# Kernel tuning notes

Hardware: AMD Instinct MI355X
Metric: run time of the kernel (lower is better)

## Reference

```python
import jax, jax.numpy as jnp
import numpy as np

NUM_CLASSES = 80
FOCAL_ALPHA = 0.25
FOCAL_GAMMA = 2.0
HUBER_SIGMA = 3.0
REG_MEAN = 0.0
REG_STD = 0.2
IMG_H = 800.0
IMG_W = 800.0
B, A, M = 4, 100000, 32


def setup_inputs() -> dict:
    key = jax.random.key(0)
    k1, k2, k3, k4, k5, k6, k7 = jax.random.split(key, 7)
    classification = jax.random.uniform(k1, (B, A, NUM_CLASSES), dtype=jnp.float32)
    regression = jax.random.normal(k2, (B, A, 4), dtype=jnp.float32)
    # plausible anchors: centers inside image, sizes 16..256
    cx = jax.random.uniform(k3, (A,), minval=0.0, maxval=IMG_W)
    cy = jax.random.uniform(k4, (A,), minval=0.0, maxval=IMG_H)
    s = jax.random.uniform(k5, (A, 2), minval=16.0, maxval=256.0)
    anchors = jnp.stack([cx - s[:, 0] / 2, cy - s[:, 1] / 2,
                         cx + s[:, 0] / 2, cy + s[:, 1] / 2], axis=1).astype(jnp.float32)
    # annotations: [B, M, 5] = x1,y1,x2,y2,class
    xy = jax.random.uniform(k6, (B, M, 2), minval=0.0, maxval=650.0)
    wh = jax.random.uniform(k7, (B, M, 2), minval=30.0, maxval=150.0)
    cls = jax.random.randint(jax.random.fold_in(key, 9), (B, M, 1), 0, NUM_CLASSES).astype(jnp.float32)
    annotations = jnp.concatenate([xy, xy + wh, cls], axis=-1)
    return {"classification": classification, "regression": regression,
            "anchors": anchors, "annotations": annotations}


def _pairwise_iou(anchors, boxes):
    # anchors [A,4], boxes [M,4] -> [A,M]
    ix1 = jnp.maximum(anchors[:, None, 0], boxes[None, :, 0])
    iy1 = jnp.maximum(anchors[:, None, 1], boxes[None, :, 1])
    ix2 = jnp.minimum(anchors[:, None, 2], boxes[None, :, 2])
    iy2 = jnp.minimum(anchors[:, None, 3], boxes[None, :, 3])
    inter = jnp.clip(ix2 - ix1, 0.0) * jnp.clip(iy2 - iy1, 0.0)
    area_a = (anchors[:, 2] - anchors[:, 0]) * (anchors[:, 3] - anchors[:, 1])
    area_b = (boxes[:, 2] - boxes[:, 0]) * (boxes[:, 3] - boxes[:, 1])
    union = area_a[:, None] + area_b[None, :] - inter
    return inter / jnp.maximum(union, 1e-8)


def _targets(anchors, annotations):
    # per-image anchor assignment, vmapped over batch
    def per_image(ann):
        boxes = ann[:, :4]
        cls = ann[:, 4].astype(jnp.int32)
        ious = _pairwise_iou(anchors, boxes)          # [A,M]
        best = jnp.argmax(ious, axis=1)               # [A]
        best_iou = jnp.max(ious, axis=1)
        pos = best_iou >= 0.5
        ign = (best_iou > 0.4) & (~pos)
        states = jnp.where(pos, 1.0, jnp.where(ign, -1.0, 0.0))
        cx = (anchors[:, 0] + anchors[:, 2]) * 0.5
        cy = (anchors[:, 1] + anchors[:, 3]) * 0.5
        inside = (cx >= 0) & (cx < IMG_W) & (cy >= 0) & (cy < IMG_H)
        states = jnp.where(inside, states, -1.0)
        labels = jax.nn.one_hot(cls[best], NUM_CLASSES, dtype=jnp.float32) * pos[:, None]
        ab = boxes[best]                              # assigned gt boxes [A,4]
        aw = anchors[:, 2] - anchors[:, 0]
        ah = anchors[:, 3] - anchors[:, 1]
        t = jnp.stack([(ab[:, 0] - anchors[:, 0]) / aw,
                       (ab[:, 1] - anchors[:, 1]) / ah,
                       (ab[:, 2] - anchors[:, 2]) / aw,
                       (ab[:, 3] - anchors[:, 3]) / ah], axis=1)
        t = (t - REG_MEAN) / REG_STD
        return labels, t, states
    return jax.vmap(per_image)(annotations)


def reference(classification, regression, anchors, annotations):
    labels, reg_t, states = _targets(anchors, annotations)   # [B,A,K],[B,A,4],[B,A]
    num_pos = jnp.maximum(jnp.sum((states == 1.0).astype(jnp.float32)), 1.0)
    # focal loss over non-ignored anchors
    valid = (states != -1.0)[..., None].astype(jnp.float32)
    p = jnp.clip(classification, 1e-4, 1.0 - 1e-4)
    bce = -(labels * jnp.log(p) + (1.0 - labels) * jnp.log1p(-p))
    alpha_f = jnp.where(labels == 1.0, FOCAL_ALPHA, 1.0 - FOCAL_ALPHA)
    focal_w = alpha_f * jnp.where(labels == 1.0, 1.0 - p, p) ** FOCAL_GAMMA
    cls_loss = jnp.sum(focal_w * bce * valid) / num_pos
    # smooth L1 over positive anchors
    pos_m = (states == 1.0)[..., None].astype(jnp.float32)
    s2 = HUBER_SIGMA ** 2
    d = jnp.abs(regression - reg_t)
    l1 = jnp.where(d < 1.0 / s2, 0.5 * s2 * d * d, d - 0.5 / s2)
    reg_loss = jnp.sum(l1 * pos_m) / num_pos
    return cls_loss + reg_loss
```

## Files before the change

kernel.cpp:

```cpp
#include <hip/hip_runtime.h>

#define BB 4
#define AA 100000
#define MM 32
#define NC 80
#define GX 391
#define NBLK (GX * BB)


#define FOCAL_K(vk, flatk)                                                  \
  {                                                                         \
    const int s    = (flatk) / 20;                                          \
    const int colb = ((flatk) - s * 20) * 4;                                \
    const int c    = scode[s];                                              \
    const float m  = (c != -2) ? 1.0f : 0.0f;                               \
    const float q0 = fminf(fmaxf((vk).x, 1e-4f), 0.9999f);                  \
    const float q1 = fminf(fmaxf((vk).y, 1e-4f), 0.9999f);                  \
    const float q2 = fminf(fmaxf((vk).z, 1e-4f), 0.9999f);                  \
    const float q3 = fminf(fmaxf((vk).w, 1e-4f), 0.9999f);                  \
    float sub = 0.0f;                                                       \
    sub += 0.75f * q0 * q0 * (-__logf(1.0f - q0));                          \
    sub += 0.75f * q1 * q1 * (-__logf(1.0f - q1));                          \
    sub += 0.75f * q2 * q2 * (-__logf(1.0f - q2));                          \
    sub += 0.75f * q3 * q3 * (-__logf(1.0f - q3));                          \
    csum += m * sub;                                                        \
    const unsigned rel = (unsigned)(c - colb);                              \
    if (rel < 4u) {      \
      const float p = (rel & 2u) ? ((rel & 1u) ? q3 : q2)                   \
                                 : ((rel & 1u) ? q1 : q0);                  \
      const float onem = 1.0f - p;                                          \
      csum += 0.25f * onem * onem * (-__logf(p))                            \
            - 0.75f * p * p * (-__logf(onem));                              \
    }                                                                       \
  }

#define FOCAL_BATCH(vv, batch)                                              \
  _Pragma("unroll")                                                         \
  for (int k = 0; k < 5; ++k) {                                             \
    const int flat = ((batch) * 5 + k) * 256 + tid;                         \
    FOCAL_K((vv)[k], flat)                                                  \
  }

__global__ __launch_bounds__(256, 4) void fused_kernel(
    const float* __restrict__ anchors,
    const float* __restrict__ annotations,
    const float* __restrict__ regression,
    const float* __restrict__ cls,
    float* __restrict__ cls_part,
    float* __restrict__ reg_part,
    unsigned* __restrict__ pos_part)
{
    __shared__ float ann[MM * 5];
    __shared__ float areab[MM];
    __shared__ int scode[256];
    const int b = blockIdx.y;
    const int tid = threadIdx.x;
    if (tid < MM * 5) ann[tid] = annotations[b * MM * 5 + tid];
    if (tid < MM) {
        const float bx1 = annotations[b * MM * 5 + tid * 5 + 0];
        const float by1 = annotations[b * MM * 5 + tid * 5 + 1];
        const float bx2 = annotations[b * MM * 5 + tid * 5 + 2];
        const float by2 = annotations[b * MM * 5 + tid * 5 + 3];
        areab[tid] = __fmul_rn(__fsub_rn(bx2, bx1), __fsub_rn(by2, by1));
    }
    __syncthreads();

    const int abase = blockIdx.x * 256;
    const int a = abase + tid;

    const float4* base4 = (const float4*)cls + ((size_t)b * AA + abase) * 20;
    const int maxflat = (abase + 256 <= AA) ? (5120 - 1) : ((AA - abase) * 20 - 1);

    float4 vA[5], vB[5];
    #pragma unroll
    for (int k = 0; k < 5; ++k) vA[k] = base4[min(k * 256 + tid, maxflat)];
    #pragma unroll
    for (int k = 0; k < 5; ++k) vB[k] = base4[min((5 + k) * 256 + tid, maxflat)];
    __builtin_amdgcn_sched_barrier(0);

    float reg_sum = 0.0f;
    int pos_cnt = 0;
    int code = -2;

    if (a < AA) {
        const float4 an = ((const float4*)anchors)[a];
        const float ax1 = an.x, ay1 = an.y, ax2 = an.z, ay2 = an.w;
        const float area_a = __fmul_rn(__fsub_rn(ax2, ax1), __fsub_rn(ay2, ay1));

        float best_iou = -1.0f;
        int best = 0;
        #pragma unroll
        for (int j = 0; j < MM; ++j) {
            const float bx1 = ann[j * 5 + 0];
            const float by1 = ann[j * 5 + 1];
            const float bx2 = ann[j * 5 + 2];
            const float by2 = ann[j * 5 + 3];
            const float ix1 = fmaxf(ax1, bx1);
            const float iy1 = fmaxf(ay1, by1);
            const float ix2 = fminf(ax2, bx2);
            const float iy2 = fminf(ay2, by2);
            const float iw = fmaxf(__fsub_rn(ix2, ix1), 0.0f);
            const float ih = fmaxf(__fsub_rn(iy2, iy1), 0.0f);
            const float inter = __fmul_rn(iw, ih);
            const float uni = __fsub_rn(__fadd_rn(area_a, areab[j]), inter);
            const float iou = __fdiv_rn(inter, fmaxf(uni, 1e-8f));
            if (iou > best_iou) { best_iou = iou; best = j; }
        }

        const bool pos = best_iou >= 0.5f;
        const bool ign = (best_iou > 0.4f) && !pos;
        const float cx = (ax1 + ax2) * 0.5f;
        const float cy = (ay1 + ay2) * 0.5f;
        const bool inside = (cx >= 0.0f) && (cx < 800.0f) && (cy >= 0.0f) && (cy < 800.0f);

        const bool valid = inside && !ign;
        if (valid) code = pos ? (int)ann[best * 5 + 4] : -1;

        if (pos && inside) {
            pos_cnt = 1;
            const float aw = ax2 - ax1;
            const float ah = ay2 - ay1;
            const float bx1 = ann[best * 5 + 0];
            const float by1 = ann[best * 5 + 1];
            const float bx2 = ann[best * 5 + 2];
            const float by2 = ann[best * 5 + 3];
            float t[4];
            t[0] = ((bx1 - ax1) / aw) / 0.2f;
            t[1] = ((by1 - ay1) / ah) / 0.2f;
            t[2] = ((bx2 - ax2) / aw) / 0.2f;
            t[3] = ((by2 - ay2) / ah) / 0.2f;
            const float* rg = regression + (((size_t)b * AA + a) * 4);
            #pragma unroll
            for (int k = 0; k < 4; ++k) {
                const float d = fabsf(rg[k] - t[k]);
                reg_sum += (d < (1.0f / 9.0f)) ? (4.5f * d * d) : (d - (0.5f / 9.0f));
            }
        }
    }
    scode[tid] = code;
    __syncthreads();

    float csum = 0.0f;

    float4 vC[5];
    #pragma unroll
    for (int k = 0; k < 5; ++k) vC[k] = base4[min((10 + k) * 256 + tid, maxflat)];

    FOCAL_BATCH(vA, 0)

    float4 vD[5];
    #pragma unroll
    for (int k = 0; k < 5; ++k) vD[k] = base4[min((15 + k) * 256 + tid, maxflat)];

    FOCAL_BATCH(vB, 1)
    FOCAL_BATCH(vC, 2)
    FOCAL_BATCH(vD, 3)

    #pragma unroll
    for (int off = 32; off > 0; off >>= 1) {
        csum    += __shfl_down(csum, off);
        reg_sum += __shfl_down(reg_sum, off);
        pos_cnt += __shfl_down(pos_cnt, off);
    }
    __shared__ float wc[4], wr[4];
    __shared__ int   wp[4];
    const int wave = tid >> 6, lane = tid & 63;
    if (lane == 0) { wc[wave] = csum; wr[wave] = reg_sum; wp[wave] = pos_cnt; }
    __syncthreads();
    if (tid == 0) {
        const int idx = b * GX + blockIdx.x;
        cls_part[idx] = wc[0] + wc[1] + wc[2] + wc[3];
        reg_part[idx] = wr[0] + wr[1] + wr[2] + wr[3];
        pos_part[idx] = (unsigned)(wp[0] + wp[1] + wp[2] + wp[3]);
    }
}

__global__ __launch_bounds__(256) void finalize_kernel(
    const float* __restrict__ cls_part,
    const float* __restrict__ reg_part,
    const unsigned* __restrict__ pos_part,
    float* __restrict__ out)
{
    float cs = 0.0f, rs = 0.0f;
    unsigned pc = 0;
    for (int i = threadIdx.x; i < NBLK; i += 256) {
        cs += cls_part[i];
        rs += reg_part[i];
        pc += pos_part[i];
    }
    #pragma unroll
    for (int off = 32; off > 0; off >>= 1) {
        cs += __shfl_down(cs, off);
        rs += __shfl_down(rs, off);
        pc += __shfl_down(pc, off);
    }
    __shared__ float wc[4], wr[4];
    __shared__ unsigned wp[4];
    const int wave = threadIdx.x >> 6, lane = threadIdx.x & 63;
    if (lane == 0) { wc[wave] = cs; wr[wave] = rs; wp[wave] = pc; }
    __syncthreads();
    if (threadIdx.x == 0) {
        const float csum = wc[0] + wc[1] + wc[2] + wc[3];
        const float rsum = wr[0] + wr[1] + wr[2] + wr[3];
        const float np = fmaxf((float)(wp[0] + wp[1] + wp[2] + wp[3]), 1.0f);
        out[0] = (csum + rsum) / np;
    }
}

extern "C" void kernel_launch(void* const* d_in, const int* in_sizes, int n_in,
                              void* d_out, int out_size, void* d_ws, size_t ws_size,
                              hipStream_t stream)
{
    const float* classification = (const float*)d_in[0];
    const float* regression     = (const float*)d_in[1];
    const float* anchors        = (const float*)d_in[2];
    const float* annotations    = (const float*)d_in[3];
    float* out = (float*)d_out;

    float*    cls_part = (float*)d_ws;
    float*    reg_part = cls_part + NBLK;
    unsigned* pos_part = (unsigned*)(reg_part + NBLK);

    dim3 grid(GX, BB);
    fused_kernel<<<grid, 256, 0, stream>>>(anchors, annotations, regression,
                                           classification, cls_part, reg_part, pos_part);
    finalize_kernel<<<1, 256, 0, stream>>>(cls_part, reg_part, pos_part, out);
}
```

Before: 209.7 us.

## Prefetch first classification chunk via global_load_lds instead of registers

Replaces the two register-held prefetch batches with a direct global-to-LDS async load of the first batch, staged in a 20KB shared buffer, and issues later batch loads in a software-pipelined order. It also drops the min-blocks-per-SM hint from launch bounds. The aim is to overlap the classification stream with the IoU assignment phase while freeing registers. In exchange it uses more LDS per block, which may reduce occupancy. It relies on the implicit barrier before the focal phase to make the LDS writes visible.

```diff
diff --git a/kernel.cpp b/kernel.cpp
--- a/kernel.cpp
+++ b/kernel.cpp
@@ -7,6 +7,13 @@
 #define GX 391
 #define NBLK (GX * BB)
 
+
+__device__ __forceinline__ void gld_lds16(const float4* g, float4* l) {
+    __builtin_amdgcn_global_load_lds(
+        (const __attribute__((address_space(1))) void*)g,
+        (__attribute__((address_space(3))) void*)l,
+        16, 0, 0);
+}
 
 #define FOCAL_K(vk, flatk)                                                  \
   {                                                                         \
@@ -41,7 +48,7 @@
     FOCAL_K((vv)[k], flat)                                                  \
   }
 
-__global__ __launch_bounds__(256, 4) void fused_kernel(
+__global__ __launch_bounds__(256) void fused_kernel(
     const float* __restrict__ anchors,
     const float* __restrict__ annotations,
     const float* __restrict__ regression,
@@ -53,6 +60,7 @@
     __shared__ float ann[MM * 5];
     __shared__ float areab[MM];
     __shared__ int scode[256];
+    __shared__ float4 pre[5 * 256];
     const int b = blockIdx.y;
     const int tid = threadIdx.x;
     if (tid < MM * 5) ann[tid] = annotations[b * MM * 5 + tid];
@@ -67,23 +75,21 @@
 
     const int abase = blockIdx.x * 256;
     const int a = abase + tid;
-
     const float4* base4 = (const float4*)cls + ((size_t)b * AA + abase) * 20;
     const int maxflat = (abase + 256 <= AA) ? (5120 - 1) : ((AA - abase) * 20 - 1);
 
-    float4 vA[5], vB[5];
-    #pragma unroll
-    for (int k = 0; k < 5; ++k) vA[k] = base4[min(k * 256 + tid, maxflat)];
-    #pragma unroll
-    for (int k = 0; k < 5; ++k) vB[k] = base4[min((5 + k) * 256 + tid, maxflat)];
-    __builtin_amdgcn_sched_barrier(0);
+    float4 an = make_float4(0.f, 0.f, 0.f, 0.f);
+    if (a < AA) an = ((const float4*)anchors)[a];
+
+    #pragma unroll
+    for (int k = 0; k < 5; ++k)
+        gld_lds16(&base4[min(k * 256 + tid, maxflat)], &pre[k * 256 + tid]);
 
     float reg_sum = 0.0f;
     int pos_cnt = 0;
     int code = -2;
 
     if (a < AA) {
-        const float4 an = ((const float4*)anchors)[a];
         const float ax1 = an.x, ay1 = an.y, ax2 = an.z, ay2 = an.w;
         const float area_a = __fmul_rn(__fsub_rn(ax2, ax1), __fsub_rn(ay2, ay1));
 
@@ -142,19 +148,25 @@
 
     float csum = 0.0f;
 
-    float4 vC[5];
-    #pragma unroll
-    for (int k = 0; k < 5; ++k) vC[k] = base4[min((10 + k) * 256 + tid, maxflat)];
-
-    FOCAL_BATCH(vA, 0)
-
-    float4 vD[5];
-    #pragma unroll
-    for (int k = 0; k < 5; ++k) vD[k] = base4[min((15 + k) * 256 + tid, maxflat)];
-
-    FOCAL_BATCH(vB, 1)
-    FOCAL_BATCH(vC, 2)
-    FOCAL_BATCH(vD, 3)
+    float4 v1[5];
+    #pragma unroll
+    for (int k = 0; k < 5; ++k) v1[k] = base4[min((5 + k) * 256 + tid, maxflat)];
+
+    float4 v0[5];
+    #pragma unroll
+    for (int k = 0; k < 5; ++k) v0[k] = pre[k * 256 + tid];
+    FOCAL_BATCH(v0, 0)
+
+    float4 v2[5];
+    #pragma unroll
+    for (int k = 0; k < 5; ++k) v2[k] = base4[min((10 + k) * 256 + tid, maxflat)];
+    FOCAL_BATCH(v1, 1)
+
+    float4 v3[5];
+    #pragma unroll
+    for (int k = 0; k < 5; ++k) v3[k] = base4[min((15 + k) * 256 + tid, maxflat)];
+    FOCAL_BATCH(v2, 2)
+    FOCAL_BATCH(v3, 3)
 
     #pragma unroll
     for (int off = 32; off > 0; off >>= 1) {
```

After: 196.8 us (median of 2 runs). 6.1% less time.
